# Kernel optimization log

Measured on AMD Instinct MI355X. Metric: run time of the kernel, lower is better.

## Reference

```python
import jax, jax.numpy as jnp
import numpy as np

INPUT_DIMS = 512
OUTPUT_DIMS = 512
GRID_SIZE = 8


def setup_inputs() -> dict:
    key = jax.random.key(0)
    k_x, k_w = jax.random.split(key)
    x = jax.random.normal(k_x, (4, 2048, INPUT_DIMS), dtype=jnp.float32)
    scale = 1.0 / (np.sqrt(INPUT_DIMS) * np.sqrt(GRID_SIZE))
    fouriercoeffs = jax.random.normal(
        k_w, (2, OUTPUT_DIMS, INPUT_DIMS, GRID_SIZE), dtype=jnp.float32) * scale
    bias = jnp.zeros((1, OUTPUT_DIMS), dtype=jnp.float32)
    return {"x": x, "fouriercoeffs": fouriercoeffs, "bias": bias}


def reference(x, fouriercoeffs, bias):
    out_shape = x.shape[:-1] + (OUTPUT_DIMS,)
    xf = x.reshape(-1, INPUT_DIMS)  # [N, I]
    k = jnp.arange(1, GRID_SIZE + 1, dtype=x.dtype)  # [G]
    arg = xf[:, :, None] * k  # [N, I, G]
    # contract cos/sin features against coeffs: two batched GEMMs
    y = jnp.einsum('nig,oig->no', jnp.cos(arg), fouriercoeffs[0])
    y = y + jnp.einsum('nig,oig->no', jnp.sin(arg), fouriercoeffs[1])
    y = y + bias
    return y.reshape(out_shape)
```

## Files before the change

### kernel.cpp

```cpp
#include <hip/hip_runtime.h>
#include <hip/hip_bf16.h>


typedef __attribute__((ext_vector_type(8))) short s16x8;
typedef __attribute__((ext_vector_type(4))) int   i32x4;
typedef __attribute__((ext_vector_type(4))) float f32x4;

#define NROWS 8192
#define IDIM  512
#define ODIM  512
#define KDIM  8192

static __device__ __forceinline__ short f2bf(float f) {
    union { float f; unsigned u; } v; v.f = f;
    unsigned r = v.u + 0x7fffu + ((v.u >> 16) & 1u);
    return (short)(r >> 16);
}

static __device__ __forceinline__ float bf2f(short h) {
    union { unsigned u; float f; } v;
    v.u = ((unsigned)(unsigned short)h) << 16;
    return v.f;
}

static __device__ __forceinline__ int pkbf(float c, float s) {
    union { __hip_bfloat162 h; int i; } u;
    u.h = __float22bfloat162_rn(make_float2(c, s));
    return u.i;
}

__global__ __launch_bounds__(256) void fkan_prep(const float* __restrict__ cf,
                                                 short* __restrict__ Wb) {
    const int o = blockIdx.x;
    const int tid = threadIdx.x;
#pragma unroll
    for (int rep = 0; rep < 2; ++rep) {
        const int i = tid + rep * 256;
        const float* c0 = cf + (o * 512 + i) * 8;
        const float* c1 = cf + ((512 + o) * 512 + i) * 8;
        float4 a0 = *(const float4*)c0;
        float4 a1 = *(const float4*)(c0 + 4);
        float4 b0 = *(const float4*)c1;
        float4 b1 = *(const float4*)(c1 + 4);
        s16x8 lo, hi;
        lo[0] = f2bf(a0.x); lo[1] = f2bf(b0.x);
        lo[2] = f2bf(a0.y); lo[3] = f2bf(b0.y);
        lo[4] = f2bf(a0.z); lo[5] = f2bf(b0.z);
        lo[6] = f2bf(a0.w); lo[7] = f2bf(b0.w);
        hi[0] = f2bf(a1.x); hi[1] = f2bf(b1.x);
        hi[2] = f2bf(a1.y); hi[3] = f2bf(b1.y);
        hi[4] = f2bf(a1.z); hi[5] = f2bf(b1.z);
        hi[6] = f2bf(a1.w); hi[7] = f2bf(b1.w);
        *(s16x8*)(Wb + o * KDIM + i * 16)     = lo;
        *(s16x8*)(Wb + o * KDIM + i * 16 + 8) = hi;
    }
}

template <int KSPLIT>
__global__ __launch_bounds__(256, 2) void fkan_gemm(const float* __restrict__ x,
                                                    const short* __restrict__ Wb,
                                                    const float* __restrict__ bias,
                                                    void* __restrict__ outp) {
    __shared__ short As[2][128 * 64];
    __shared__ short Bs[2][128 * 64];

    const int bid = blockIdx.x;
    int bn, kc, bm;
    if (KSPLIT == 2) {
        const int xcd = bid & 7;
        bn = xcd & 3; kc = xcd >> 2; bm = bid >> 3;
    } else {
        const int xcd = bid & 7, idx = bid >> 3;
        bn = xcd & 3; kc = 0; bm = idx + (xcd >> 2) * 32;
    }
    const int n0 = bm * 128, o0 = bn * 128;
    const int NKT = 128 / KSPLIT;
    const int i0 = kc * (512 / KSPLIT);
    const int kbase = i0 * 16;

    const int tid = threadIdx.x;
    const int wid = tid >> 6, lane = tid & 63;
    const int lrow = lane & 15, lk = lane >> 4;
    const int wr = wid >> 1, wc = wid & 1;

    f32x4 acc[4][4];
#pragma unroll
    for (int a = 0; a < 4; ++a)
#pragma unroll
        for (int b = 0; b < 4; ++b) {
            f32x4 z = {0.f, 0.f, 0.f, 0.f};
            acc[a][b] = z;
        }

    const int nl = tid >> 1, isel = tid & 1;
    const float* xrow = x + (n0 + nl) * 512 + i0 + isel * 2;

    auto stage = [&](int t, int nb, float2 xvv) {
#pragma unroll
        for (int w = 0; w < 4; ++w) {
            const int chunk = w * 256 + tid;
            const int r = chunk >> 3, pc = chunk & 7;
            const int lc = pc ^ (r & 7);
            const short* src = Wb + (o0 + r) * KDIM + kbase + t * 64 + lc * 8;
            short* ldst = &Bs[nb][w * 2048 + wid * 512];
            __builtin_amdgcn_global_load_lds(
                (const __attribute__((address_space(1))) void*)src,
                (__attribute__((address_space(3))) void*)ldst, 16, 0, 0);
        }
#pragma unroll
        for (int ii = 0; ii < 2; ++ii) {
            const float xx = ii ? xvv.y : xvv.x;
            float s1, c1;
            __sincosf(xx, &s1, &c1);
            float c = c1, s = s1;
            i32x4 lo, hi;
#pragma unroll
            for (int g = 0; g < 8; ++g) {
                const int p = pkbf(c, s);
                if (g < 4) lo[g] = p; else hi[g - 4] = p;
                const float t1 = s * s1, t2 = c * s1;
                const float cn = __builtin_fmaf(c, c1, -t1);
                s = __builtin_fmaf(s, c1, t2);
                c = cn;
            }
            const int il = isel * 2 + ii;
            const int cb0 = il * 2;
            *(i32x4*)&As[nb][nl * 64 + ((cb0 ^ (nl & 7))) * 8]       = lo;
            *(i32x4*)&As[nb][nl * 64 + (((cb0 + 1) ^ (nl & 7))) * 8] = hi;
        }
    };

    float2 xv = *(const float2*)xrow;
    stage(0, 0, xv);
    xv = *(const float2*)(xrow + 4);
    __syncthreads();

    for (int kt = 0; kt < NKT; ++kt) {
        const int cur = kt & 1;
        const short* Ab = As[cur];
        const short* Bb = Bs[cur];

        s16x8 af[2][4], bfr[2][4];
#pragma unroll
        for (int ksub = 0; ksub < 2; ++ksub) {
#pragma unroll
            for (int mf = 0; mf < 4; ++mf) {
                const int row = wr * 64 + mf * 16 + lrow;
                af[ksub][mf] = *(const s16x8*)&Ab[row * 64 + ((ksub * 4 + lk) ^ (row & 7)) * 8];
            }
#pragma unroll
            for (int nf = 0; nf < 4; ++nf) {
                const int row = wc * 64 + nf * 16 + lrow;
                bfr[ksub][nf] = *(const s16x8*)&Bb[row * 64 + ((ksub * 4 + lk) ^ (row & 7)) * 8];
            }
        }

        if (kt + 1 < NKT) {
            stage(kt + 1, cur ^ 1, xv);
            if (kt + 2 < NKT) xv = *(const float2*)(xrow + (kt + 2) * 4);
        }

        __builtin_amdgcn_s_setprio(1);
#pragma unroll
        for (int ksub = 0; ksub < 2; ++ksub)
#pragma unroll
            for (int mf = 0; mf < 4; ++mf)
#pragma unroll
                for (int nf = 0; nf < 4; ++nf)
                    acc[mf][nf] = __builtin_amdgcn_mfma_f32_16x16x32_bf16(
                        af[ksub][mf], bfr[ksub][nf], acc[mf][nf], 0, 0, 0);
        __builtin_amdgcn_s_setprio(0);

        __syncthreads();
    }

    if (KSPLIT == 2) {
        unsigned short* dst = (unsigned short*)outp + (size_t)kc * (NROWS * ODIM);
#pragma unroll
        for (int nf = 0; nf < 4; ++nf) {
            const int oc = o0 + wc * 64 + nf * 16 + lrow;
#pragma unroll
            for (int mf = 0; mf < 4; ++mf) {
                const f32x4 v = acc[mf][nf];
                const int rbase = n0 + wr * 64 + mf * 16 + lk * 4;
#pragma unroll
                for (int j = 0; j < 4; ++j)
                    dst[(size_t)(rbase + j) * 512 + oc] = (unsigned short)f2bf(v[j]);
            }
        }
    } else {
        float* dst = (float*)outp;
#pragma unroll
        for (int nf = 0; nf < 4; ++nf) {
            const int oc = o0 + wc * 64 + nf * 16 + lrow;
            const float bv = bias[oc];
#pragma unroll
            for (int mf = 0; mf < 4; ++mf) {
                const f32x4 v = acc[mf][nf];
                const int rbase = n0 + wr * 64 + mf * 16 + lk * 4;
#pragma unroll
                for (int j = 0; j < 4; ++j)
                    dst[(size_t)(rbase + j) * 512 + oc] = v[j] + bv;
            }
        }
    }
}

__global__ __launch_bounds__(256) void fkan_combine(const short* __restrict__ P,
                                                    const float* __restrict__ bias,
                                                    float* __restrict__ out) {
    const int total = NROWS * ODIM;
    const int stride = gridDim.x * 256 * 8;
    for (int e = (blockIdx.x * 256 + threadIdx.x) * 8; e < total; e += stride) {
        s16x8 a = *(const s16x8*)(P + e);
        s16x8 b = *(const s16x8*)(P + total + e);
        const int col = e & 511;
        float4 c0 = *(const float4*)(bias + col);
        float4 c1 = *(const float4*)(bias + col + 4);
        float4 r0, r1;
        r0.x = bf2f(a[0]) + bf2f(b[0]) + c0.x;
        r0.y = bf2f(a[1]) + bf2f(b[1]) + c0.y;
        r0.z = bf2f(a[2]) + bf2f(b[2]) + c0.z;
        r0.w = bf2f(a[3]) + bf2f(b[3]) + c0.w;
        r1.x = bf2f(a[4]) + bf2f(b[4]) + c1.x;
        r1.y = bf2f(a[5]) + bf2f(b[5]) + c1.y;
        r1.z = bf2f(a[6]) + bf2f(b[6]) + c1.z;
        r1.w = bf2f(a[7]) + bf2f(b[7]) + c1.w;
        *(float4*)(out + e)     = r0;
        *(float4*)(out + e + 4) = r1;
    }
}

extern "C" void kernel_launch(void* const* d_in, const int* in_sizes, int n_in,
                              void* d_out, int out_size, void* d_ws, size_t ws_size,
                              hipStream_t stream) {
    const float* x    = (const float*)d_in[0];
    const float* cf   = (const float*)d_in[1];
    const float* bias = (const float*)d_in[2];
    float* out = (float*)d_out;

    const size_t partial_bytes = (size_t)2 * NROWS * ODIM * 2;
    const size_t wb_bytes = (size_t)ODIM * KDIM * 2;

    if (ws_size >= partial_bytes + wb_bytes) {
        short* P  = (short*)d_ws;
        short* Wb = (short*)((char*)d_ws + partial_bytes);
        fkan_prep<<<512, 256, 0, stream>>>(cf, Wb);
        fkan_gemm<2><<<512, 256, 0, stream>>>(x, Wb, bias, (void*)P);
        fkan_combine<<<2048, 256, 0, stream>>>(P, bias, out);
    } else {
        short* Wb = (short*)d_ws;
        fkan_prep<<<512, 256, 0, stream>>>(cf, Wb);
        fkan_gemm<1><<<256, 256, 0, stream>>>(x, Wb, bias, (void*)out);
    }
}
```

Measured before the change: 102.3 us.

## Switch to 4-way K split with full-width 128x512 tiles and 512-thread blocks

The main GEMM now has each block cover all 512 output columns for 128 rows, with a 4-way split over the input dimension instead of 2-way split with 128x128 tiles. Each row's sin/cos features are then computed once per block instead of once per output-column tile, which cuts the redundant transcendental work and A-tile staging. The cost is twice as many bf16 partials to write and read in the combine step, larger per-thread accumulators (register pressure), more shared memory, and extra bf16 rounding error across four partials.

```diff
diff --git a/kernel.cpp b/kernel.cpp
--- a/kernel.cpp
+++ b/kernel.cpp
@@ -56,52 +56,184 @@
     }
 }
 
-template <int KSPLIT>
-__global__ __launch_bounds__(256, 2) void fkan_gemm(const float* __restrict__ x,
-                                                    const short* __restrict__ Wb,
-                                                    const float* __restrict__ bias,
-                                                    void* __restrict__ outp) {
+__global__ __launch_bounds__(512, 2) void fkan_gemm4(const float* __restrict__ x,
+                                                     const short* __restrict__ Wb,
+                                                     short* __restrict__ P) {
+    __shared__ short As[2][128 * 64];
+    __shared__ short Bs[2][256 * 64];
+
+    const int bid = blockIdx.x;
+    const int xcd = bid & 7;
+    const int kc  = xcd >> 1;
+    const int bm  = ((bid >> 3) << 1) | (xcd & 1);
+    const int n0 = bm * 128;
+    const int i0 = kc * 128;
+    const int kbase = i0 * 16;
+    const int NKT = 64;
+
+    const int tid = threadIdx.x;
+    const int wid = tid >> 6, lane = tid & 63;
+    const int lrow = lane & 15, lk = lane >> 4;
+    const int wr = wid >> 2, wc = wid & 3;
+
+    f32x4 acc[4][8];
+#pragma unroll
+    for (int a = 0; a < 4; ++a)
+#pragma unroll
+        for (int b = 0; b < 8; ++b) {
+            f32x4 z = {0.f, 0.f, 0.f, 0.f};
+            acc[a][b] = z;
+        }
+
+    const int nl = tid >> 2, isel = tid & 3;
+    const float* xrow = x + (n0 + nl) * 512 + i0 + isel;
+
+    auto stageA = [&](short* Ab, float xx) {
+        float s1, c1;
+        __sincosf(xx, &s1, &c1);
+        float c = c1, s = s1;
+        i32x4 lo, hi;
+#pragma unroll
+        for (int g = 0; g < 8; ++g) {
+            const int p = pkbf(c, s);
+            if (g < 4) lo[g] = p; else hi[g - 4] = p;
+            const float t1 = s * s1, t2 = c * s1;
+            const float cn = __builtin_fmaf(c, c1, -t1);
+            s = __builtin_fmaf(s, c1, t2);
+            c = cn;
+        }
+        const int cb0 = isel * 2;
+        *(i32x4*)&Ab[nl * 64 + ((cb0 ^ (nl & 7))) * 8]       = lo;
+        *(i32x4*)&Ab[nl * 64 + (((cb0 + 1) ^ (nl & 7))) * 8] = hi;
+    };
+
+    auto stageB = [&](int t, int nb) {
+#pragma unroll
+        for (int w = 0; w < 4; ++w) {
+            const int ch = w * 512 + tid;
+            const int l = ch >> 3, sl = ch & 7;
+            const int cb = sl ^ (l & 7);
+            const int r = 2 * l + (cb >> 2);
+            const short* src = Wb + (size_t)r * KDIM + kbase + t * 32 + (cb & 3) * 8;
+            short* ldst = &Bs[nb][w * 4096 + wid * 512];
+            __builtin_amdgcn_global_load_lds(
+                (const __attribute__((address_space(1))) void*)src,
+                (__attribute__((address_space(3))) void*)ldst, 16, 0, 0);
+        }
+    };
+
+    float xv = xrow[0];
+    stageA(As[0], xv);
+    stageB(0, 0);
+    xv = xrow[4];
+    __syncthreads();
+
+    for (int kt = 0; kt < NKT; ++kt) {
+        const int bcur = kt & 1;
+        const int abuf = (kt >> 1) & 1;
+
+        s16x8 af[4], bfr[8];
+#pragma unroll
+        for (int mf = 0; mf < 4; ++mf) {
+            const int row = wr * 64 + mf * 16 + lrow;
+            af[mf] = *(const s16x8*)&As[abuf][row * 64 + (((kt & 1) * 4 + lk) ^ (row & 7)) * 8];
+        }
+#pragma unroll
+        for (int nf = 0; nf < 8; ++nf) {
+            const int r = wc * 128 + nf * 16 + lrow;
+            const int l = r >> 1;
+            const int sl = (((r & 1) * 4 + lk) ^ (l & 7));
+            bfr[nf] = *(const s16x8*)&Bs[bcur][l * 64 + sl * 8];
+        }
+
+        if (kt + 1 < NKT) stageB(kt + 1, bcur ^ 1);
+        if ((kt & 1) == 0 && kt + 2 < NKT) {
+            stageA(As[abuf ^ 1], xv);
+            if (kt + 4 < NKT) xv = xrow[((kt >> 1) + 2) * 4];
+        }
+
+        __builtin_amdgcn_s_setprio(1);
+#pragma unroll
+        for (int mf = 0; mf < 4; ++mf)
+#pragma unroll
+            for (int nf = 0; nf < 8; ++nf)
+                acc[mf][nf] = __builtin_amdgcn_mfma_f32_16x16x32_bf16(
+                    af[mf], bfr[nf], acc[mf][nf], 0, 0, 0);
+        __builtin_amdgcn_s_setprio(0);
+
+        __syncthreads();
+    }
+
+    unsigned short* dst = (unsigned short*)P + (size_t)kc * (NROWS * ODIM);
+#pragma unroll
+    for (int nf = 0; nf < 8; ++nf) {
+        const int oc = wc * 128 + nf * 16 + lrow;
+#pragma unroll
+        for (int mf = 0; mf < 4; ++mf) {
+            const f32x4 v = acc[mf][nf];
+            const int rbase = n0 + wr * 64 + mf * 16 + lk * 4;
+#pragma unroll
+            for (int j = 0; j < 4; ++j)
+                dst[(size_t)(rbase + j) * 512 + oc] = (unsigned short)f2bf(v[j]);
+        }
+    }
+}
+
+__global__ __launch_bounds__(256) void fkan_combine4(const short* __restrict__ P,
+                                                     const float* __restrict__ bias,
+                                                     float* __restrict__ out) {
+    const int total = NROWS * ODIM;
+    const int stride = gridDim.x * 256 * 8;
+    for (int e = (blockIdx.x * 256 + threadIdx.x) * 8; e < total; e += stride) {
+        s16x8 a = *(const s16x8*)(P + e);
+        s16x8 b = *(const s16x8*)(P + total + e);
+        s16x8 c = *(const s16x8*)(P + 2 * total + e);
+        s16x8 d = *(const s16x8*)(P + 3 * total + e);
+        const int col = e & 511;
+        float4 c0 = *(const float4*)(bias + col);
+        float4 c1 = *(const float4*)(bias + col + 4);
+        float4 r0, r1;
+        r0.x = (bf2f(a[0]) + bf2f(b[0])) + (bf2f(c[0]) + bf2f(d[0])) + c0.x;
+        r0.y = (bf2f(a[1]) + bf2f(b[1])) + (bf2f(c[1]) + bf2f(d[1])) + c0.y;
+        r0.z = (bf2f(a[2]) + bf2f(b[2])) + (bf2f(c[2]) + bf2f(d[2])) + c0.z;
+        r0.w = (bf2f(a[3]) + bf2f(b[3])) + (bf2f(c[3]) + bf2f(d[3])) + c0.w;
+        r1.x = (bf2f(a[4]) + bf2f(b[4])) + (bf2f(c[4]) + bf2f(d[4])) + c1.x;
+        r1.y = (bf2f(a[5]) + bf2f(b[5])) + (bf2f(c[5]) + bf2f(d[5])) + c1.y;
+        r1.z = (bf2f(a[6]) + bf2f(b[6])) + (bf2f(c[6]) + bf2f(d[6])) + c1.z;
+        r1.w = (bf2f(a[7]) + bf2f(b[7])) + (bf2f(c[7]) + bf2f(d[7])) + c1.w;
+        *(float4*)(out + e)     = r0;
+        *(float4*)(out + e + 4) = r1;
+    }
+}
+
+__global__ __launch_bounds__(256, 2) void fkan_gemm_fb(const float* __restrict__ x,
+                                                       const short* __restrict__ Wb,
+                                                       const float* __restrict__ bias,
+                                                       float* __restrict__ outp) {
     __shared__ short As[2][128 * 64];
     __shared__ short Bs[2][128 * 64];
-
     const int bid = blockIdx.x;
-    int bn, kc, bm;
-    if (KSPLIT == 2) {
-        const int xcd = bid & 7;
-        bn = xcd & 3; kc = xcd >> 2; bm = bid >> 3;
-    } else {
-        const int xcd = bid & 7, idx = bid >> 3;
-        bn = xcd & 3; kc = 0; bm = idx + (xcd >> 2) * 32;
-    }
+    const int xcd = bid & 7, idx = bid >> 3;
+    const int bn = xcd & 3, bm = idx + (xcd >> 2) * 32;
     const int n0 = bm * 128, o0 = bn * 128;
-    const int NKT = 128 / KSPLIT;
-    const int i0 = kc * (512 / KSPLIT);
-    const int kbase = i0 * 16;
-
     const int tid = threadIdx.x;
     const int wid = tid >> 6, lane = tid & 63;
     const int lrow = lane & 15, lk = lane >> 4;
     const int wr = wid >> 1, wc = wid & 1;
-
     f32x4 acc[4][4];
 #pragma unroll
     for (int a = 0; a < 4; ++a)
 #pragma unroll
-        for (int b = 0; b < 4; ++b) {
-            f32x4 z = {0.f, 0.f, 0.f, 0.f};
-            acc[a][b] = z;
-        }
-
+        for (int b = 0; b < 4; ++b) { f32x4 z = {0,0,0,0}; acc[a][b] = z; }
     const int nl = tid >> 1, isel = tid & 1;
-    const float* xrow = x + (n0 + nl) * 512 + i0 + isel * 2;
-
+    const float* xrow = x + (n0 + nl) * 512 + isel * 2;
     auto stage = [&](int t, int nb, float2 xvv) {
 #pragma unroll
         for (int w = 0; w < 4; ++w) {
             const int chunk = w * 256 + tid;
             const int r = chunk >> 3, pc = chunk & 7;
             const int lc = pc ^ (r & 7);
-            const short* src = Wb + (o0 + r) * KDIM + kbase + t * 64 + lc * 8;
+            const short* src = Wb + (o0 + r) * KDIM + t * 64 + lc * 8;
             short* ldst = &Bs[nb][w * 2048 + wid * 512];
             __builtin_amdgcn_global_load_lds(
                 (const __attribute__((address_space(1))) void*)src,
@@ -110,8 +242,7 @@
 #pragma unroll
         for (int ii = 0; ii < 2; ++ii) {
             const float xx = ii ? xvv.y : xvv.x;
-            float s1, c1;
-            __sincosf(xx, &s1, &c1);
+            float s1, c1; __sincosf(xx, &s1, &c1);
             float c = c1, s = s1;
             i32x4 lo, hi;
 #pragma unroll
@@ -120,47 +251,37 @@
                 if (g < 4) lo[g] = p; else hi[g - 4] = p;
                 const float t1 = s * s1, t2 = c * s1;
                 const float cn = __builtin_fmaf(c, c1, -t1);
-                s = __builtin_fmaf(s, c1, t2);
-                c = cn;
+                s = __builtin_fmaf(s, c1, t2); c = cn;
             }
-            const int il = isel * 2 + ii;
-            const int cb0 = il * 2;
+            const int cb0 = (isel * 2 + ii) * 2;
             *(i32x4*)&As[nb][nl * 64 + ((cb0 ^ (nl & 7))) * 8]       = lo;
             *(i32x4*)&As[nb][nl * 64 + (((cb0 + 1) ^ (nl & 7))) * 8] = hi;
         }
     };
-
     float2 xv = *(const float2*)xrow;
     stage(0, 0, xv);
     xv = *(const float2*)(xrow + 4);
     __syncthreads();
-
-    for (int kt = 0; kt < NKT; ++kt) {
+    for (int kt = 0; kt < 128; ++kt) {
         const int cur = kt & 1;
-        const short* Ab = As[cur];
-        const short* Bb = Bs[cur];
-
         s16x8 af[2][4], bfr[2][4];
 #pragma unroll
         for (int ksub = 0; ksub < 2; ++ksub) {
 #pragma unroll
             for (int mf = 0; mf < 4; ++mf) {
                 const int row = wr * 64 + mf * 16 + lrow;
-                af[ksub][mf] = *(const s16x8*)&Ab[row * 64 + ((ksub * 4 + lk) ^ (row & 7)) * 8];
+                af[ksub][mf] = *(const s16x8*)&As[cur][row * 64 + ((ksub * 4 + lk) ^ (row & 7)) * 8];
             }
 #pragma unroll
             for (int nf = 0; nf < 4; ++nf) {
                 const int row = wc * 64 + nf * 16 + lrow;
-                bfr[ksub][nf] = *(const s16x8*)&Bb[row * 64 + ((ksub * 4 + lk) ^ (row & 7)) * 8];
+                bfr[ksub][nf] = *(const s16x8*)&Bs[cur][row * 64 + ((ksub * 4 + lk) ^ (row & 7)) * 8];
             }
         }
-
-        if (kt + 1 < NKT) {
+        if (kt + 1 < 128) {
             stage(kt + 1, cur ^ 1, xv);
-            if (kt + 2 < NKT) xv = *(const float2*)(xrow + (kt + 2) * 4);
-        }
-
-        __builtin_amdgcn_s_setprio(1);
+            if (kt + 2 < 128) xv = *(const float2*)(xrow + (kt + 2) * 4);
+        }
 #pragma unroll
         for (int ksub = 0; ksub < 2; ++ksub)
 #pragma unroll
@@ -169,65 +290,20 @@
                 for (int nf = 0; nf < 4; ++nf)
                     acc[mf][nf] = __builtin_amdgcn_mfma_f32_16x16x32_bf16(
                         af[ksub][mf], bfr[ksub][nf], acc[mf][nf], 0, 0, 0);
-        __builtin_amdgcn_s_setprio(0);
-
         __syncthreads();
     }
-
-    if (KSPLIT == 2) {
-        unsigned short* dst = (unsigned short*)outp + (size_t)kc * (NROWS * ODIM);
-#pragma unroll
-        for (int nf = 0; nf < 4; ++nf) {
-            const int oc = o0 + wc * 64 + nf * 16 + lrow;
-#pragma unroll
-            for (int mf = 0; mf < 4; ++mf) {
-                const f32x4 v = acc[mf][nf];
-                const int rbase = n0 + wr * 64 + mf * 16 + lk * 4;
-#pragma unroll
-                for (int j = 0; j < 4; ++j)
-                    dst[(size_t)(rbase + j) * 512 + oc] = (unsigned short)f2bf(v[j]);
-            }
-        }
-    } else {
-        float* dst = (float*)outp;
-#pragma unroll
-        for (int nf = 0; nf < 4; ++nf) {
-            const int oc = o0 + wc * 64 + nf * 16 + lrow;
-            const float bv = bias[oc];
-#pragma unroll
-            for (int mf = 0; mf < 4; ++mf) {
-                const f32x4 v = acc[mf][nf];
-                const int rbase = n0 + wr * 64 + mf * 16 + lk * 4;
-#pragma unroll
-                for (int j = 0; j < 4; ++j)
-                    dst[(size_t)(rbase + j) * 512 + oc] = v[j] + bv;
-            }
-        }
-    }
-}
-
-__global__ __launch_bounds__(256) void fkan_combine(const short* __restrict__ P,
-                                                    const float* __restrict__ bias,
-                                                    float* __restrict__ out) {
-    const int total = NROWS * ODIM;
-    const int stride = gridDim.x * 256 * 8;
-    for (int e = (blockIdx.x * 256 + threadIdx.x) * 8; e < total; e += stride) {
-        s16x8 a = *(const s16x8*)(P + e);
-        s16x8 b = *(const s16x8*)(P + total + e);
-        const int col = e & 511;
-        float4 c0 = *(const float4*)(bias + col);
-        float4 c1 = *(const float4*)(bias + col + 4);
-        float4 r0, r1;
-        r0.x = bf2f(a[0]) + bf2f(b[0]) + c0.x;
-        r0.y = bf2f(a[1]) + bf2f(b[1]) + c0.y;
-        r0.z = bf2f(a[2]) + bf2f(b[2]) + c0.z;
-        r0.w = bf2f(a[3]) + bf2f(b[3]) + c0.w;
-        r1.x = bf2f(a[4]) + bf2f(b[4]) + c1.x;
-        r1.y = bf2f(a[5]) + bf2f(b[5]) + c1.y;
-        r1.z = bf2f(a[6]) + bf2f(b[6]) + c1.z;
-        r1.w = bf2f(a[7]) + bf2f(b[7]) + c1.w;
-        *(float4*)(out + e)     = r0;
-        *(float4*)(out + e + 4) = r1;
+#pragma unroll
+    for (int nf = 0; nf < 4; ++nf) {
+        const int oc = o0 + wc * 64 + nf * 16 + lrow;
+        const float bv = bias[oc];
+#pragma unroll
+        for (int mf = 0; mf < 4; ++mf) {
+            const f32x4 v = acc[mf][nf];
+            const int rbase = n0 + wr * 64 + mf * 16 + lk * 4;
+#pragma unroll
+            for (int j = 0; j < 4; ++j)
+                outp[(size_t)(rbase + j) * 512 + oc] = v[j] + bv;
+        }
     }
 }
 
@@ -239,18 +315,18 @@
     const float* bias = (const float*)d_in[2];
     float* out = (float*)d_out;
 
-    const size_t partial_bytes = (size_t)2 * NROWS * ODIM * 2;
+    const size_t partial_bytes = (size_t)4 * NROWS * ODIM * 2;
     const size_t wb_bytes = (size_t)ODIM * KDIM * 2;
 
     if (ws_size >= partial_bytes + wb_bytes) {
         short* P  = (short*)d_ws;
         short* Wb = (short*)((char*)d_ws + partial_bytes);
         fkan_prep<<<512, 256, 0, stream>>>(cf, Wb);
-        fkan_gemm<2><<<512, 256, 0, stream>>>(x, Wb, bias, (void*)P);
-        fkan_combine<<<2048, 256, 0, stream>>>(P, bias, out);
+        fkan_gemm4<<<256, 512, 0, stream>>>(x, Wb, P);
+        fkan_combine4<<<2048, 256, 0, stream>>>(P, bias, out);
     } else {
         short* Wb = (short*)d_ws;
         fkan_prep<<<512, 256, 0, stream>>>(cf, Wb);
-        fkan_gemm<1><<<256, 256, 0, stream>>>(x, Wb, bias, (void*)out);
-    }
-}
+        fkan_gemm_fb<<<256, 256, 0, stream>>>(x, Wb, bias, out);
+    }
+}
```

Result: faster. 92.56 us (-9.5%).
